# Optimization experiments

Measured on AMD Instinct MI355X. Metric: run time of the kernel, lower is better.

## Reference

```python
import jax, jax.numpy as jnp
import numpy as np

D_MODEL = 256
NHEAD = 8
D_HEAD = D_MODEL // NHEAD


def setup_inputs() -> dict:
    key = jax.random.key(0)
    ks = jax.random.split(key, 5)
    s = 0.02
    return {
        "x": jax.random.normal(ks[0], (2, 4096, D_MODEL), dtype=jnp.float32),
        "source": jax.random.normal(ks[1], (2, 6144, D_MODEL), dtype=jnp.float32),
        "Wq": jax.random.normal(ks[2], (D_MODEL, D_MODEL), dtype=jnp.float32) * s,
        "Wk": jax.random.normal(ks[3], (D_MODEL, D_MODEL), dtype=jnp.float32) * s,
        "Wv": jax.random.normal(ks[4], (D_MODEL, D_MODEL), dtype=jnp.float32) * s,
    }


def reference(x, source, Wq, Wk, Wv):
    B, L1, D = x.shape
    L2 = source.shape[1]
    scale = D_HEAD ** (-0.5)
    # torch Linear: y = x @ W.T  (W is [out, in])
    q = (x @ Wq.T).reshape(B, L1, NHEAD, D_HEAD)
    k = (source @ Wk.T).reshape(B, L2, NHEAD, D_HEAD)
    v = (source @ Wv.T).reshape(B, L2, NHEAD, D_HEAD)
    # scores: [B, H, L1, L2]
    attn = jnp.einsum("bqhd,bkhd->bhqk", q, k) * scale
    attn = jax.nn.softmax(attn, axis=-1)
    out = jnp.einsum("bhqk,bkhd->bqhd", attn, v)
    return out.reshape(B, L1, D)
```

## Files before the change

kernel.cpp:

```cpp
#include <hip/hip_runtime.h>
#include <math.h>

#define B_   2
#define L1_  4096
#define L2_  6144
#define DM_  256
#define H_   8
#define DH_  32

typedef __bf16 bf16x8 __attribute__((ext_vector_type(8)));
typedef __bf16 bf16x4 __attribute__((ext_vector_type(4)));
typedef float floatx4 __attribute__((ext_vector_type(4)));
typedef _Float16 f16;
typedef _Float16 f16x4 __attribute__((ext_vector_type(4)));
typedef _Float16 f16x8 __attribute__((ext_vector_type(8)));
typedef __fp16 fp16v2 __attribute__((ext_vector_type(2)));

__device__ __forceinline__ bf16x8 ldb(const __bf16* p) { return *(const bf16x8*)p; }

__device__ __forceinline__ bf16x4 pack4(floatx4 v) {
    bf16x4 r;
    r[0] = (__bf16)v[0]; r[1] = (__bf16)v[1];
    r[2] = (__bf16)v[2]; r[3] = (__bf16)v[3];
    return r;
}

__device__ __forceinline__ float pkrtz(float a, float b) {
    fp16v2 p = __builtin_amdgcn_cvt_pkrtz(a, b);
    return __builtin_bit_cast(float, p);
}

__global__ __launch_bounds__(256) void cvt_all(
    const float* __restrict__ wq, const float* __restrict__ wk,
    const float* __restrict__ wv, const float* __restrict__ x,
    const float* __restrict__ src,
    __bf16* __restrict__ wbf, __bf16* __restrict__ xbf, __bf16* __restrict__ sbf,
    float qscale)
{
    int i = blockIdx.x * 256 + threadIdx.x;
    const float* s; __bf16* d; float sc = 1.0f; size_t off;
    if (i < 49152) {
        int seg = i >> 14;
        off = (size_t)(i & 16383) * 4;
        s = seg == 0 ? wq : (seg == 1 ? wk : wv);
        d = wbf + (size_t)seg * 65536;
        if (seg == 0) sc = qscale;
    } else if (i < 49152 + 524288) {
        off = (size_t)(i - 49152) * 4; s = x; d = xbf;
    } else {
        off = (size_t)(i - 49152 - 524288) * 4; s = src; d = sbf;
    }
    float4 v = *(const float4*)(s + off);
    bf16x4 r;
    r[0] = (__bf16)(v.x * sc); r[1] = (__bf16)(v.y * sc);
    r[2] = (__bf16)(v.z * sc); r[3] = (__bf16)(v.w * sc);
    *(bf16x4*)(d + off) = r;
}

__global__ __launch_bounds__(256) void proj_kernel(
    const __bf16* __restrict__ xbf, const __bf16* __restrict__ sbf,
    const __bf16* __restrict__ Wbf,
    __bf16* __restrict__ qo, __bf16* __restrict__ ko, f16* __restrict__ vo)
{
    __shared__ f16 ldsV[256 * 36];

    const int bid = blockIdx.x;
    int y, xb;
    if      (bid < 256) { y = 0; xb = bid; }
    else if (bid < 640) { y = 1; xb = bid - 256; }
    else                { y = 2; xb = bid - 640; }

    const int L = (y == 0) ? L1_ : L2_;
    const __bf16* X   = (y == 0) ? xbf : sbf;
    const __bf16* Wb  = Wbf + (size_t)y * 65536;

    const int lane = threadIdx.x & 63;
    const int w    = threadIdx.x >> 6;
    const int g    = lane >> 4;
    const int c    = lane & 15;
    const int mb   = xb * 32;
    const int b    = mb / L;
    const int lb   = mb - b * L;

    floatx4 acc[2][4];
#pragma unroll
    for (int s = 0; s < 2; s++)
#pragma unroll
        for (int n = 0; n < 4; n++) acc[s][n] = (floatx4){0.f, 0.f, 0.f, 0.f};

#pragma unroll
    for (int kc = 0; kc < 8; kc++) {
        bf16x8 xf0 = ldb(X + (size_t)(mb + c) * DM_ + kc * 32 + g * 8);
        bf16x8 xf1 = ldb(X + (size_t)(mb + 16 + c) * DM_ + kc * 32 + g * 8);
#pragma unroll
        for (int n = 0; n < 4; n++) {
            const int oc = w * 64 + n * 16 + c;
            bf16x8 wf = ldb(Wb + (size_t)oc * DM_ + kc * 32 + g * 8);
            if (y == 2) {
                acc[0][n] = __builtin_amdgcn_mfma_f32_16x16x32_bf16(xf0, wf, acc[0][n], 0, 0, 0);
                acc[1][n] = __builtin_amdgcn_mfma_f32_16x16x32_bf16(xf1, wf, acc[1][n], 0, 0, 0);
            } else {
                acc[0][n] = __builtin_amdgcn_mfma_f32_16x16x32_bf16(wf, xf0, acc[0][n], 0, 0, 0);
                acc[1][n] = __builtin_amdgcn_mfma_f32_16x16x32_bf16(wf, xf1, acc[1][n], 0, 0, 0);
            }
        }
    }

    const int bhb = b * H_;
    if (y == 2) {
#pragma unroll
        for (int s = 0; s < 2; s++)
#pragma unroll
            for (int n = 0; n < 4; n++) {
                int dg = w * 64 + (n >> 1) * 32 + (n & 1) * 16 + c;
                int ll = s * 16 + g * 4;
                float2 pr;
                pr.x = pkrtz(acc[s][n][0], acc[s][n][1]);
                pr.y = pkrtz(acc[s][n][2], acc[s][n][3]);
                *(float2*)(ldsV + (size_t)dg * 36 + ll) = pr;
            }
        __syncthreads();
        const int t = threadIdx.x;
        f16* row = vo + ((size_t)(bhb + (t >> 5)) * DH_ + (t & 31)) * (size_t)L + lb;
#pragma unroll
        for (int j = 0; j < 4; j++)
            *(f16x8*)(row + j * 8) = *(const f16x8*)(ldsV + (size_t)t * 36 + j * 8);
    } else {
        __bf16* out = (y == 0) ? qo : ko;
#pragma unroll
        for (int s = 0; s < 2; s++)
#pragma unroll
            for (int n = 0; n < 4; n++) {
                int dlo = (n & 1) * 16 + g * 4;
                int h = w * 2 + (n >> 1);
                int l = lb + s * 16 + c;
                *(bf16x4*)(out + ((size_t)(bhb + h) * (size_t)L + l) * DH_ + dlo) = pack4(acc[s][n]);
            }
    }
}

template<bool DIRECT>
__global__ __launch_bounds__(256, 2) void attn_kernel(
    const __bf16* __restrict__ Q, const __bf16* __restrict__ K,
    const f16* __restrict__ VT, float* __restrict__ out,
    f16* __restrict__ Opart, float* __restrict__ Lpart, int klen, int split)
{
    __shared__ f16 ldsP[4][2][1024];

    const int bid  = blockIdx.x;
    const int work = (bid & 7) * (32 * split) + (bid >> 3);
    const int xb   = work & 15;
    const int bh   = (work >> 4) & 15;
    const int z    = work >> 8;

    const int lane  = threadIdx.x & 63;
    const int w     = threadIdx.x >> 6;
    const int g     = lane >> 4;
    const int c     = lane & 15;
    const int qbase = xb * 256 + w * 64;
    const int k0    = z * klen;

    bf16x8 qf[4];
#pragma unroll
    for (int h = 0; h < 4; h++)
        qf[h] = ldb(Q + ((size_t)bh * L1_ + qbase + h * 16 + c) * DH_ + g * 8);

    const __bf16* kbase = K  + (size_t)bh * L2_ * DH_ + (size_t)c * DH_ + g * 8;
    const f16*    vb0   = VT + ((size_t)bh * DH_ + c)      * L2_ + g * 8;
    const f16*    vb1   = VT + ((size_t)bh * DH_ + 16 + c) * L2_ + g * 8;
    f16* Pw = &ldsP[w][0][0];

    float l[4] = {0.f, 0.f, 0.f, 0.f};
    floatx4 o[4][2];
#pragma unroll
    for (int h = 0; h < 4; h++) { o[h][0] = (floatx4){0.f,0.f,0.f,0.f}; o[h][1] = (floatx4){0.f,0.f,0.f,0.f}; }

#pragma unroll 1
    for (int t = 0; t < klen; t += 64) {
        const int kb = k0 + t;
        bf16x8 kf[4];
        kf[0] = ldb(kbase + (size_t)kb * DH_);
        kf[1] = ldb(kbase + (size_t)(kb + 16) * DH_);
        kf[2] = ldb(kbase + (size_t)(kb + 32) * DH_);
        kf[3] = ldb(kbase + (size_t)(kb + 48) * DH_);
        f16x8 vf[4];
        vf[0] = *(const f16x8*)(vb0 + kb);
        vf[1] = *(const f16x8*)(vb1 + kb);
        vf[2] = *(const f16x8*)(vb0 + kb + 32);
        vf[3] = *(const f16x8*)(vb1 + kb + 32);

#pragma unroll
        for (int hp = 0; hp < 2; hp++) {
#pragma unroll
            for (int hh = 0; hh < 2; hh++) {
                const int h = hp * 2 + hh;
                floatx4 s[4];
#pragma unroll
                for (int st = 0; st < 4; st++)
                    s[st] = __builtin_amdgcn_mfma_f32_16x16x32_bf16(
                                kf[st], qf[h], (floatx4){0.f, 0.f, 0.f, 0.f}, 0, 0, 0);
#pragma unroll
                for (int st = 0; st < 4; st++) {
                    float e0 = __builtin_amdgcn_exp2f(s[st][0]);
                    float e1 = __builtin_amdgcn_exp2f(s[st][1]);
                    float e2 = __builtin_amdgcn_exp2f(s[st][2]);
                    float e3 = __builtin_amdgcn_exp2f(s[st][3]);
                    l[h] += (e0 + e1) + (e2 + e3);
                    float2 pr;
                    pr.x = pkrtz(e0, e1);
                    pr.y = pkrtz(e2, e3);
                    *(float2*)(Pw + hh * 1024 + ((st * 2 + (g >> 1)) * 16 + c) * 8 + (g & 1) * 4) = pr;
                }
            }
#pragma unroll
            for (int kc = 0; kc < 2; kc++)
#pragma unroll
                for (int hh = 0; hh < 2; hh++) {
                    const int h = hp * 2 + hh;
                    f16x8 pa = *(const f16x8*)(Pw + hh * 1024 + ((kc * 4 + g) * 16 + c) * 8);
                    o[h][0] = __builtin_amdgcn_mfma_f32_16x16x32_f16(pa, vf[kc * 2 + 0], o[h][0], 0, 0, 0);
                    o[h][1] = __builtin_amdgcn_mfma_f32_16x16x32_f16(pa, vf[kc * 2 + 1], o[h][1], 0, 0, 0);
                }
        }
    }

#pragma unroll
    for (int h = 0; h < 4; h++) {
        l[h] += __shfl_xor(l[h], 16, 64);
        l[h] += __shfl_xor(l[h], 32, 64);
    }

    const int b  = bh / H_;
    const int hh = bh % H_;
    if (DIRECT) {
#pragma unroll
        for (int h = 0; h < 4; h++)
#pragma unroll
            for (int r = 0; r < 4; r++) {
                float lr  = __shfl(l[h], g * 4 + r, 64);
                float inv = 1.0f / lr;
                size_t base = ((size_t)(b * L1_ + qbase + h * 16 + g * 4 + r)) * DM_ + hh * DH_;
                out[base + c]      = o[h][0][r] * inv;
                out[base + 16 + c] = o[h][1][r] * inv;
            }
    } else {
        f16* Op = Opart + (size_t)z * ((size_t)B_ * L1_ * DM_);
#pragma unroll
        for (int h = 0; h < 4; h++) {
#pragma unroll
            for (int r = 0; r < 4; r++) {
                size_t base = ((size_t)(b * L1_ + qbase + h * 16 + g * 4 + r)) * DM_ + hh * DH_;
                Op[base + c]      = (f16)o[h][0][r];
                Op[base + 16 + c] = (f16)o[h][1][r];
            }
            if (g == 0)
                Lpart[(size_t)z * ((size_t)B_ * H_ * L1_) +
                      (size_t)bh * L1_ + qbase + h * 16 + c] = l[h];
        }
    }
}

__global__ __launch_bounds__(256) void combine_kernel(
    const f16* __restrict__ Opart, const float* __restrict__ Lpart,
    float* __restrict__ out, int split)
{
    int t   = blockIdx.x * 256 + threadIdx.x;
    int row = t >> 6;
    int col = (t & 63) * 4;
    int b   = row >> 12;
    int q   = row & (L1_ - 1);
    int bh  = b * H_ + (col >> 5);
    float4 a = {0.f, 0.f, 0.f, 0.f};
    float ls = 0.f;
    for (int z = 0; z < split; z++) {
        const f16* Op = Opart + (size_t)z * ((size_t)B_ * L1_ * DM_);
        f16x4 v = *(const f16x4*)(Op + (size_t)row * DM_ + col);
        a.x += (float)v[0]; a.y += (float)v[1];
        a.z += (float)v[2]; a.w += (float)v[3];
        ls += Lpart[(size_t)z * ((size_t)B_ * H_ * L1_) + (size_t)bh * L1_ + q];
    }
    float inv = 1.0f / ls;
    float4 r; r.x = a.x * inv; r.y = a.y * inv; r.z = a.z * inv; r.w = a.w * inv;
    *(float4*)(out + (size_t)row * DM_ + col) = r;
}

extern "C" void kernel_launch(void* const* d_in, const int* in_sizes, int n_in,
                              void* d_out, int out_size, void* d_ws, size_t ws_size,
                              hipStream_t stream) {
    const float* x   = (const float*)d_in[0];
    const float* src = (const float*)d_in[1];
    const float* Wq  = (const float*)d_in[2];
    const float* Wk  = (const float*)d_in[3];
    const float* Wv  = (const float*)d_in[4];
    float* out = (float*)d_out;

    const float qscale = 1.4426950408889634f / sqrtf((float)DH_);

    const size_t nW = 3 * 65536;
    const size_t nQ = (size_t)B_ * H_ * L1_ * DH_;
    const size_t nK = (size_t)B_ * H_ * L2_ * DH_;
    const size_t nX = nQ;

    __bf16* wbf = (__bf16*)d_ws;
    __bf16* qws = wbf + nW;
    __bf16* kws = qws + nQ;
    f16*    vt  = (f16*)(kws + nK);
    size_t unionOff = ((nW + nQ + 2 * nK) * 2 + 255) & ~(size_t)255;
    __bf16* xbf = (__bf16*)((char*)d_ws + unionOff);
    __bf16* sbf = xbf + nX;

    const size_t oPartB = (size_t)B_ * L1_ * DM_ * sizeof(f16);
    const size_t lPartB = (size_t)B_ * H_ * L1_ * 4;
    const size_t avail  = ws_size > unionOff ? ws_size - unionOff : 0;
    int split = 1;
    if      (avail >= 8 * (oPartB + lPartB)) split = 8;
    else if (avail >= 6 * (oPartB + lPartB)) split = 6;
    else if (avail >= 4 * (oPartB + lPartB)) split = 4;
    else if (avail >= 2 * (oPartB + lPartB)) split = 2;
    f16*   Opart = (f16*)((char*)d_ws + unionOff);
    float* Lpart = (float*)((char*)d_ws + unionOff + (size_t)split * oPartB);

    cvt_all<<<dim3(5312), 256, 0, stream>>>(Wq, Wk, Wv, x, src, wbf, xbf, sbf, qscale);
    proj_kernel<<<dim3(1024), 256, 0, stream>>>(xbf, sbf, wbf, qws, kws, vt);

    if (split > 1) {
        attn_kernel<false><<<dim3(256 * split), 256, 0, stream>>>(
            qws, kws, vt, nullptr, Opart, Lpart, L2_ / split, split);
        combine_kernel<<<dim3(2048), 256, 0, stream>>>(Opart, Lpart, out, split);
    } else {
        attn_kernel<true><<<dim3(256), 256, 0, stream>>>(
            qws, kws, vt, out, nullptr, nullptr, L2_, 1);
    }
}
```

Before: 195.2 us.

## Stage K/V tiles through double-buffered LDS shared across waves

Each wave used to load its own K and V fragments straight from global memory every iteration. Now the four waves cooperatively load one 64-key K/V tile into padded LDS buffers. The next tile is prefetched into registers while the current one is computed, then written into the alternate buffer. This cuts redundant global loads by four, at the cost of a block-wide barrier per iteration and more LDS use, which may reduce occupancy.

```diff
diff --git a/kernel.cpp b/kernel.cpp
--- a/kernel.cpp
+++ b/kernel.cpp
@@ -7,6 +7,13 @@
 #define DM_  256
 #define H_   8
 #define DH_  32
+
+#define KROW 80
+#define VROW 144
+#define KBUF (64 * KROW)
+#define VBUF (32 * VROW)
+#define POFF (2 * KBUF + 2 * VBUF)
+#define LDSZ (POFF + 4 * 4096)
 
 typedef __bf16 bf16x8 __attribute__((ext_vector_type(8)));
 typedef __bf16 bf16x4 __attribute__((ext_vector_type(4)));
@@ -121,7 +128,8 @@
             }
         __syncthreads();
         const int t = threadIdx.x;
-        f16* row = vo + ((size_t)(bhb + (t >> 5)) * DH_ + (t & 31)) * (size_t)L + lb;
+        const int h = t >> 5, d = t & 31;
+        f16* row = vo + ((size_t)(bhb + h) * DH_ + d) * (size_t)L + lb;
 #pragma unroll
         for (int j = 0; j < 4; j++)
             *(f16x8*)(row + j * 8) = *(const f16x8*)(ldsV + (size_t)t * 36 + j * 8);
@@ -145,7 +153,7 @@
     const f16* __restrict__ VT, float* __restrict__ out,
     f16* __restrict__ Opart, float* __restrict__ Lpart, int klen, int split)
 {
-    __shared__ f16 ldsP[4][2][1024];
+    __shared__ __align__(16) unsigned char lds[LDSZ];
 
     const int bid  = blockIdx.x;
     const int work = (bid & 7) * (32 * split) + (bid >> 3);
@@ -165,29 +173,51 @@
     for (int h = 0; h < 4; h++)
         qf[h] = ldb(Q + ((size_t)bh * L1_ + qbase + h * 16 + c) * DH_ + g * 8);
 
-    const __bf16* kbase = K  + (size_t)bh * L2_ * DH_ + (size_t)c * DH_ + g * 8;
-    const f16*    vb0   = VT + ((size_t)bh * DH_ + c)      * L2_ + g * 8;
-    const f16*    vb1   = VT + ((size_t)bh * DH_ + 16 + c) * L2_ + g * 8;
-    f16* Pw = &ldsP[w][0][0];
+    const int krow = w * 16 + (lane >> 2);
+    const int kchk = lane & 3;
+    const int vrow = w * 8 + (lane >> 3);
+    const int vchk = lane & 7;
+    const __bf16* kgbase = K  + ((size_t)bh * L2_ + krow) * DH_ + kchk * 8;
+    const f16*    vgbase = VT + ((size_t)bh * DH_ + vrow) * L2_ + vchk * 8;
+    unsigned char* dstK = lds + krow * KROW + kchk * 16;
+    unsigned char* dstV = lds + 2 * KBUF + vrow * VROW + vchk * 16;
+    f16* Pw = (f16*)(lds + POFF + w * 4096);
 
     float l[4] = {0.f, 0.f, 0.f, 0.f};
     floatx4 o[4][2];
 #pragma unroll
     for (int h = 0; h < 4; h++) { o[h][0] = (floatx4){0.f,0.f,0.f,0.f}; o[h][1] = (floatx4){0.f,0.f,0.f,0.f}; }
 
+    {
+        float4 kr = *(const float4*)(kgbase + (size_t)k0 * DH_);
+        float4 vr = *(const float4*)(vgbase + k0);
+        *(float4*)dstK = kr;
+        *(float4*)dstV = vr;
+    }
+
+    int buf = 0;
 #pragma unroll 1
     for (int t = 0; t < klen; t += 64) {
-        const int kb = k0 + t;
+        __syncthreads();
+
+        float4 kr, vr;
+        const bool more = (t + 64) < klen;
+        if (more) {
+            kr = *(const float4*)(kgbase + (size_t)(k0 + t + 64) * DH_);
+            vr = *(const float4*)(vgbase + (k0 + t + 64));
+        }
+
+        const unsigned char* bK = lds + buf * KBUF;
+        const unsigned char* bV = lds + 2 * KBUF + buf * VBUF;
         bf16x8 kf[4];
-        kf[0] = ldb(kbase + (size_t)kb * DH_);
-        kf[1] = ldb(kbase + (size_t)(kb + 16) * DH_);
-        kf[2] = ldb(kbase + (size_t)(kb + 32) * DH_);
-        kf[3] = ldb(kbase + (size_t)(kb + 48) * DH_);
+#pragma unroll
+        for (int st = 0; st < 4; st++)
+            kf[st] = *(const bf16x8*)(bK + (st * 16 + c) * KROW + g * 16);
         f16x8 vf[4];
-        vf[0] = *(const f16x8*)(vb0 + kb);
-        vf[1] = *(const f16x8*)(vb1 + kb);
-        vf[2] = *(const f16x8*)(vb0 + kb + 32);
-        vf[3] = *(const f16x8*)(vb1 + kb + 32);
+        vf[0] = *(const f16x8*)(bV + c * VROW + g * 16);
+        vf[1] = *(const f16x8*)(bV + (16 + c) * VROW + g * 16);
+        vf[2] = *(const f16x8*)(bV + c * VROW + 64 + g * 16);
+        vf[3] = *(const f16x8*)(bV + (16 + c) * VROW + 64 + g * 16);
 
 #pragma unroll
         for (int hp = 0; hp < 2; hp++) {
@@ -222,6 +252,12 @@
                     o[h][1] = __builtin_amdgcn_mfma_f32_16x16x32_f16(pa, vf[kc * 2 + 1], o[h][1], 0, 0, 0);
                 }
         }
+
+        if (more) {
+            *(float4*)(lds + (buf ^ 1) * KBUF + krow * KROW + kchk * 16) = kr;
+            *(float4*)(lds + 2 * KBUF + (buf ^ 1) * VBUF + vrow * VROW + vchk * 16) = vr;
+        }
+        buf ^= 1;
     }
 
 #pragma unroll
```

Measured after the change: 178.8 us. 8.4% less time.
